# Performance work log

Hardware: AMD Instinct MI355X
Metric: run time of the kernel (lower is better)

The kernel has to match this reference:

```python
import jax, jax.numpy as jnp
import numpy as np

N = 50000
E = 1_600_000
D_IN = 128
D_H = 64
D_E = 32
NEG_SLOPE = 0.2


def setup_inputs() -> dict:
    key = jax.random.key(0)
    ks = jax.random.split(key, 20)
    p = lambda k, sh: jax.random.normal(k, sh, jnp.float32) * 0.1
    return {
        "x": jax.random.normal(ks[0], (N, D_IN), jnp.float32),
        "edge_index": jax.random.randint(ks[1], (2, E), 0, N, jnp.int32),
        "edge_attr": jax.random.normal(ks[2], (E, D_E), jnp.float32),
        # layer 1 params (GATv2Conv, heads=1)
        "Wl1": p(ks[3], (D_IN, D_H)), "bl1": p(ks[4], (D_H,)),
        "Wr1": p(ks[5], (D_IN, D_H)), "br1": p(ks[6], (D_H,)),
        "We1": p(ks[7], (D_E, D_H)),
        "att1": p(ks[8], (D_H,)), "bias1": p(ks[9], (D_H,)),
        # layer 2 params
        "Wl2": p(ks[10], (D_H, D_H)), "bl2": p(ks[11], (D_H,)),
        "Wr2": p(ks[12], (D_H, D_H)), "br2": p(ks[13], (D_H,)),
        "We2": p(ks[14], (D_E, D_H)),
        "att2": p(ks[15], (D_H,)), "bias2": p(ks[16], (D_H,)),
        # classifier
        "Wc": p(ks[17], (D_H, 2)), "bc": p(ks[18], (2,)),
    }


def _gatv2(x, src, dst, eattr, Wl, bl, Wr, br, We, att, bias, n):
    # x: [n, d_in]; src/dst: [Ea]; eattr: [Ea, d_e]
    xl = x @ Wl + bl                      # [n, d_h] (source transform; also message value)
    xr = x @ Wr + br                      # [n, d_h] (target transform)
    z = xl[src] + xr[dst] + eattr @ We    # [Ea, d_h]
    score = jax.nn.leaky_relu(z, NEG_SLOPE) @ att  # [Ea]
    # numerically stable softmax over incoming edges per destination node
    m = jax.ops.segment_max(score, dst, num_segments=n)
    ex = jnp.exp(score - m[dst])
    denom = jax.ops.segment_sum(ex, dst, num_segments=n)
    alpha = ex / denom[dst]               # [Ea]
    out = jax.ops.segment_sum(alpha[:, None] * xl[src], dst, num_segments=n)
    return out + bias


def reference(x, edge_index, edge_attr,
              Wl1, bl1, Wr1, br1, We1, att1, bias1,
              Wl2, bl2, Wr2, br2, We2, att2, bias2,
              Wc, bc):
    n = x.shape[0]
    src, dst = edge_index[0], edge_index[1]
    # add self-loops with fill_value='mean' (PyG default with edge_attr):
    # self-loop edge feature of node i = mean of edge_attr over edges into i
    e = edge_attr.shape[0]
    deg = jax.ops.segment_sum(jnp.ones((e,), edge_attr.dtype), dst, num_segments=n)
    loop_attr = jax.ops.segment_sum(edge_attr, dst, num_segments=n) / jnp.maximum(deg, 1.0)[:, None]
    loop = jnp.arange(n, dtype=edge_index.dtype)
    src_a = jnp.concatenate([src, loop])
    dst_a = jnp.concatenate([dst, loop])
    ea = jnp.concatenate([edge_attr, loop_attr], axis=0)

    h = jax.nn.relu(_gatv2(x, src_a, dst_a, ea, Wl1, bl1, Wr1, br1, We1, att1, bias1, n))
    # dropout(p=0.2) is identity in eval mode
    h = jax.nn.relu(_gatv2(h, src_a, dst_a, ea, Wl2, bl2, Wr2, br2, We2, att2, bias2, n))
    return h @ Wc + bc  # [n, 2]
```

## Files before the change

kernel.cpp:

```cpp
#include <hip/hip_runtime.h>
#include <hip/hip_bf16.h>

#define NEG_SLOPE 0.2f

__device__ __forceinline__ float bf2f(unsigned short u) {
    return __uint_as_float((unsigned)u << 16);
}
__device__ __forceinline__ unsigned short f2bf(float f) {
    unsigned b = __float_as_uint(f);
    return (unsigned short)((b + 0x7FFFu + ((b >> 16) & 1u)) >> 16);
}

__global__ void k_hist(const int* __restrict__ dst, int E, int* __restrict__ deg) {
    int e = blockIdx.x * 256 + threadIdx.x;
    if (e < E) atomicAdd(&deg[dst[e]], 1);
}

__global__ __launch_bounds__(1024) void k_scan_chunk(const int* __restrict__ deg,
                                                     int* __restrict__ start,
                                                     int* __restrict__ csum, int n) {
    __shared__ int wsum[16];
    const int lane = threadIdx.x & 63;
    const int w = threadIdx.x >> 6;
    int i = blockIdx.x * 1024 + (int)threadIdx.x;
    int v = (i < n) ? deg[i] : 0;
    int s = v;
#pragma unroll
    for (int o = 1; o < 64; o <<= 1) {
        int u = __shfl_up(s, o);
        if (lane >= o) s += u;
    }
    if (lane == 63) wsum[w] = s;
    __syncthreads();
    if (w == 0) {
        int ws = (lane < 16) ? wsum[lane] : 0;
#pragma unroll
        for (int o = 1; o < 16; o <<= 1) {
            int u = __shfl_up(ws, o);
            if (lane >= o) ws += u;
        }
        if (lane < 16) wsum[lane] = ws;
    }
    __syncthreads();
    int woff = (w == 0) ? 0 : wsum[w - 1];
    int incl = s + woff;
    if (i < n) start[i] = incl - v;
    if (threadIdx.x == 1023) csum[blockIdx.x] = incl;
}

__global__ void k_scan_top(int* __restrict__ csum, int nch, int* __restrict__ start, int n) {
    int t = threadIdx.x;
    int v = (t < nch) ? csum[t] : 0;
    int s = v;
#pragma unroll
    for (int o = 1; o < 64; o <<= 1) {
        int u = __shfl_up(s, o);
        if (t >= o) s += u;
    }
    if (t < nch) csum[t] = s - v;
    if (t == 63) start[n] = s;
}

__global__ void k_scan_apply(int* __restrict__ start, const int* __restrict__ csum, int n) {
    int i = blockIdx.x * 256 + threadIdx.x;
    if (i < n) start[i] += csum[i >> 10];
}

__global__ void k_fill(const int* __restrict__ src, const int* __restrict__ dst, int E,
                       const int* __restrict__ start, int* __restrict__ cursor,
                       int* __restrict__ perm, int* __restrict__ src_sorted,
                       int* __restrict__ sortpos) {
    int e = blockIdx.x * 256 + threadIdx.x;
    if (e >= E) return;
    int d = dst[e];
    int idx = start[d] + atomicAdd(&cursor[d], 1);
    perm[idx] = e;
    src_sorted[idx] = src[e];
    sortpos[e] = idx;
}

__global__ __launch_bounds__(256) void k_loop_csr(
    const float* __restrict__ eattr, const int* __restrict__ perm,
    const int* __restrict__ start, float* __restrict__ loop_attr, int n) {
    int node = blockIdx.x * 4 + (threadIdx.x >> 6);
    int t = threadIdx.x & 63;
    if (node >= n) return;
    int a = start[node], b = start[node + 1];
    int g = t >> 3, gl = t & 7;
    float4 acc = make_float4(0.f, 0.f, 0.f, 0.f);
    int j = a + g;
    for (; j + 8 < b; j += 16) {
        int e1 = perm[j];
        int e2 = perm[j + 8];
        const float4 v1 = *(const float4*)&eattr[(size_t)e1 * 32 + gl * 4];
        const float4 v2 = *(const float4*)&eattr[(size_t)e2 * 32 + gl * 4];
        acc.x += v1.x + v2.x; acc.y += v1.y + v2.y;
        acc.z += v1.z + v2.z; acc.w += v1.w + v2.w;
    }
    if (j < b) {
        int e = perm[j];
        const float4 v = *(const float4*)&eattr[(size_t)e * 32 + gl * 4];
        acc.x += v.x; acc.y += v.y; acc.z += v.z; acc.w += v.w;
    }
#pragma unroll
    for (int mask = 8; mask <= 32; mask <<= 1) {
        acc.x += __shfl_xor(acc.x, mask);
        acc.y += __shfl_xor(acc.y, mask);
        acc.z += __shfl_xor(acc.z, mask);
        acc.w += __shfl_xor(acc.w, mask);
    }
    if (t < 8) {
        float deg = fmaxf((float)(b - a), 1.f);
        float4 o = make_float4(acc.x / deg, acc.y / deg, acc.z / deg, acc.w / deg);
        *(float4*)&loop_attr[(size_t)node * 32 + gl * 4] = o;
    }
}

template <int DIN>
__global__ void k_node_transform(const float* __restrict__ h,
                                 const float* __restrict__ Wl, const float* __restrict__ bl,
                                 const float* __restrict__ Wr, const float* __restrict__ br,
                                 float* __restrict__ xl, unsigned short* __restrict__ xlb,
                                 unsigned short* __restrict__ xrb, int n) {
    __shared__ float hs[4][DIN];
    int node0 = blockIdx.x * 4;
    int tid = threadIdx.x;
    for (int idx = tid; idx < 4 * DIN; idx += 256) {
        int ln = idx / DIN, k = idx % DIN;
        int node = node0 + ln;
        hs[ln][k] = (node < n) ? h[(long long)node * DIN + k] : 0.f;
    }
    __syncthreads();
    int ln = tid >> 6;
    int j = tid & 63;
    int node = node0 + ln;
    if (node >= n) return;
    float al = bl[j], ar = br[j];
#pragma unroll 8
    for (int k = 0; k < DIN; ++k) {
        float hv = hs[ln][k];
        al += hv * Wl[k * 64 + j];
        ar += hv * Wr[k * 64 + j];
    }
    xl[(long long)node * 64 + j] = al;
    xlb[(long long)node * 64 + j] = f2bf(al);
    xrb[(long long)node * 64 + j] = f2bf(ar);
}

__global__ __launch_bounds__(256, 2) void k_edge_score(
    const unsigned short* __restrict__ xlb, const unsigned short* __restrict__ xrb,
    const float* __restrict__ eattr,
    const float* __restrict__ We, const float* __restrict__ att,
    const int* __restrict__ src, const int* __restrict__ dst,
    const int* __restrict__ sortpos, int E,
    float* __restrict__ ex_sorted) {
    __shared__ __align__(16) float We_s[32 * 64];
    __shared__ __align__(16) float ea_T[32][132];
    __shared__ float att_s[64];
    __shared__ int s_s[128], d_s[128], sp_s[128];

    const int tid = threadIdx.x;
    const int ge0 = blockIdx.x * 128;

    if (tid < 128) {
        int ge = ge0 + tid;
        bool ok = ge < E;
        s_s[tid] = ok ? src[ge] : 0;
        d_s[tid] = ok ? dst[ge] : 0;
        sp_s[tid] = ok ? sortpos[ge] : 0;
    }
    {
        const int e = tid & 127;
        const int kc = (tid >> 7) * 16;
        const int ge = ge0 + e;
        float4 a = make_float4(0.f, 0.f, 0.f, 0.f), b = a, c = a, d4 = a;
        if (ge < E) {
            const float4* p = (const float4*)(eattr + (size_t)ge * 32 + kc);
            a = p[0]; b = p[1]; c = p[2]; d4 = p[3];
        }
        ea_T[kc + 0][e] = a.x;  ea_T[kc + 1][e] = a.y;  ea_T[kc + 2][e] = a.z;  ea_T[kc + 3][e] = a.w;
        ea_T[kc + 4][e] = b.x;  ea_T[kc + 5][e] = b.y;  ea_T[kc + 6][e] = b.z;  ea_T[kc + 7][e] = b.w;
        ea_T[kc + 8][e] = c.x;  ea_T[kc + 9][e] = c.y;  ea_T[kc + 10][e] = c.z; ea_T[kc + 11][e] = c.w;
        ea_T[kc + 12][e] = d4.x; ea_T[kc + 13][e] = d4.y; ea_T[kc + 14][e] = d4.z; ea_T[kc + 15][e] = d4.w;
    }
    for (int i = tid; i < 2048; i += 256) We_s[i] = We[i];
    if (tid < 64) att_s[tid] = att[tid];
    __syncthreads();

    const int w = tid >> 6, l = tid & 63;
    const int t0 = (l & 15) * 4;
    const int e0 = w * 32 + (l >> 4) * 8;

    ushort4 xlv[8], xrv[8];
#pragma unroll
    for (int j = 0; j < 8; ++j) {
        const int eb = e0 + j;
        xlv[j] = *(const ushort4*)&xlb[(size_t)s_s[eb] * 64 + t0];
        xrv[j] = *(const ushort4*)&xrb[(size_t)d_s[eb] * 64 + t0];
    }

    float z[8][4];
#pragma unroll
    for (int j = 0; j < 8; ++j)
#pragma unroll
        for (int i = 0; i < 4; ++i) z[j][i] = 0.f;

#pragma unroll 4
    for (int k = 0; k < 32; ++k) {
        const float4 ev0 = *(const float4*)&ea_T[k][e0];
        const float4 ev1 = *(const float4*)&ea_T[k][e0 + 4];
        const float4 wv = *(const float4*)&We_s[k * 64 + t0];
        const float ee[8] = {ev0.x, ev0.y, ev0.z, ev0.w, ev1.x, ev1.y, ev1.z, ev1.w};
        const float ww[4] = {wv.x, wv.y, wv.z, wv.w};
#pragma unroll
        for (int j = 0; j < 8; ++j)
#pragma unroll
            for (int i = 0; i < 4; ++i) z[j][i] += ee[j] * ww[i];
    }

    const float4 av = *(const float4*)&att_s[t0];
    const float aa[4] = {av.x, av.y, av.z, av.w};
    float v[8];
#pragma unroll
    for (int j = 0; j < 8; ++j) {
        const float xll[4] = {bf2f(xlv[j].x), bf2f(xlv[j].y), bf2f(xlv[j].z), bf2f(xlv[j].w)};
        const float xrr[4] = {bf2f(xrv[j].x), bf2f(xrv[j].y), bf2f(xrv[j].z), bf2f(xrv[j].w)};
        float acc = 0.f;
#pragma unroll
        for (int i = 0; i < 4; ++i) {
            float zz = z[j][i] + xll[i] + xrr[i];
            zz = (zz > 0.f) ? zz : NEG_SLOPE * zz;
            acc += aa[i] * zz;
        }
        v[j] = acc;
    }
#pragma unroll
    for (int m = 1; m < 16; m <<= 1) {
#pragma unroll
        for (int j = 0; j < 8; ++j) v[j] += __shfl_xor(v[j], m);
    }
    if ((l & 15) == 0) {
#pragma unroll
        for (int j = 0; j < 8; ++j) {
            int ge = ge0 + e0 + j;
            if (ge < E) ex_sorted[sp_s[e0 + j]] = __expf(v[j]);
        }
    }
}

__global__ __launch_bounds__(256) void k_loop_score(
    const unsigned short* __restrict__ xlb, const unsigned short* __restrict__ xrb,
    const float* __restrict__ loop_attr,
    const float* __restrict__ We, const float* __restrict__ att,
    int n, float* __restrict__ ex_loop) {
    __shared__ float We_s[32 * 64];
    __shared__ float ea_T[32][68];
    __shared__ float att_s[64];

    const int tid = threadIdx.x;
    const int ge0 = blockIdx.x * 64;

    for (int i = tid; i < 2048; i += 256) We_s[i] = We[i];
    if (tid < 64) att_s[tid] = att[tid];
    {
        int e = tid & 63;
        int k0 = (tid >> 6) * 8;
        int ge = ge0 + e;
        float4 a = make_float4(0.f, 0.f, 0.f, 0.f), b = a;
        if (ge < n) {
            const float4* p = (const float4*)(loop_attr + (size_t)ge * 32 + k0);
            a = p[0]; b = p[1];
        }
        ea_T[k0 + 0][e] = a.x; ea_T[k0 + 1][e] = a.y; ea_T[k0 + 2][e] = a.z; ea_T[k0 + 3][e] = a.w;
        ea_T[k0 + 4][e] = b.x; ea_T[k0 + 5][e] = b.y; ea_T[k0 + 6][e] = b.z; ea_T[k0 + 7][e] = b.w;
    }
    __syncthreads();

    const int w = tid >> 6, l = tid & 63;
    const int t0 = (l & 15) * 4;
    const int e0 = w * 16 + (l >> 4) * 4;

    float z[4][4];
#pragma unroll
    for (int j = 0; j < 4; ++j)
#pragma unroll
        for (int i = 0; i < 4; ++i) z[j][i] = 0.f;

#pragma unroll 8
    for (int k = 0; k < 32; ++k) {
        const float4 ev = *(const float4*)&ea_T[k][e0];
        const float4 wv = *(const float4*)&We_s[k * 64 + t0];
        const float ee[4] = {ev.x, ev.y, ev.z, ev.w};
        const float ww[4] = {wv.x, wv.y, wv.z, wv.w};
#pragma unroll
        for (int j = 0; j < 4; ++j)
#pragma unroll
            for (int i = 0; i < 4; ++i) z[j][i] += ee[j] * ww[i];
    }

    const float4 av = *(const float4*)&att_s[t0];
    const float aa[4] = {av.x, av.y, av.z, av.w};
    float v[4];
#pragma unroll
    for (int j = 0; j < 4; ++j) {
        const int node = ge0 + e0 + j;
        const int nsafe = (node < n) ? node : 0;
        const ushort4 xlv = *(const ushort4*)&xlb[(size_t)nsafe * 64 + t0];
        const ushort4 xrv = *(const ushort4*)&xrb[(size_t)nsafe * 64 + t0];
        const float xll[4] = {bf2f(xlv.x), bf2f(xlv.y), bf2f(xlv.z), bf2f(xlv.w)};
        const float xrr[4] = {bf2f(xrv.x), bf2f(xrv.y), bf2f(xrv.z), bf2f(xrv.w)};
        float acc = 0.f;
#pragma unroll
        for (int i = 0; i < 4; ++i) {
            float zz = z[j][i] + xll[i] + xrr[i];
            zz = (zz > 0.f) ? zz : NEG_SLOPE * zz;
            acc += aa[i] * zz;
        }
        v[j] = acc;
    }
#pragma unroll
    for (int m = 1; m < 16; m <<= 1) {
#pragma unroll
        for (int j = 0; j < 4; ++j) v[j] += __shfl_xor(v[j], m);
    }
    if ((l & 15) == 0) {
#pragma unroll
        for (int j = 0; j < 4; ++j) {
            int node = ge0 + e0 + j;
            if (node < n) ex_loop[node] = __expf(v[j]);
        }
    }
}

template <bool FINAL>
__global__ __launch_bounds__(256, 2) void k_node_aggr(
    const float* __restrict__ xl, const int* __restrict__ start,
    const int* __restrict__ src_sorted, const float* __restrict__ ex_sorted,
    const float* __restrict__ ex_loop, const float* __restrict__ bias,
    const float* __restrict__ Wc, const float* __restrict__ bc,
    float* __restrict__ hout, int n) {
    int node = blockIdx.x * 4 + (threadIdx.x >> 6);
    int t = threadIdx.x & 63;
    if (node >= n) return;
    const int es = t >> 4;
    const int cg = t & 15;
    int a = start[node], b = start[node + 1];

    float4 acc = make_float4(0.f, 0.f, 0.f, 0.f);
    float den = 0.f;
    if (es == 0) {
        float exl = ex_loop[node];
        const float4 xv = *(const float4*)&xl[(size_t)node * 64 + cg * 4];
        acc.x = exl * xv.x; acc.y = exl * xv.y; acc.z = exl * xv.z; acc.w = exl * xv.w;
        den = exl;
    }
    for (int j = a; j < b; j += 64) {
        int m = b - j; if (m > 64) m = 64;
        int sj = 0; float exj = 0.f;
        if (t < m) { sj = src_sorted[j + t]; exj = ex_sorted[j + t]; }
        for (int i = 0; i < m; i += 16) {
            int idx[4]; float ex4[4]; const float4* p4[4];
#pragma unroll
            for (int q = 0; q < 4; ++q) {
                idx[q] = i + q * 4 + es;
                const int sq = __shfl(sj, idx[q]);
                ex4[q] = __shfl(exj, idx[q]);
                p4[q] = (const float4*)&xl[(size_t)sq * 64 + cg * 4];
            }
            float4 xv[4];
#pragma unroll
            for (int q = 0; q < 4; ++q)
                xv[q] = (idx[q] < m) ? *p4[q] : make_float4(0.f, 0.f, 0.f, 0.f);
#pragma unroll
            for (int q = 0; q < 4; ++q) {
                const float eq = (idx[q] < m) ? ex4[q] : 0.f;
                acc.x += eq * xv[q].x; acc.y += eq * xv[q].y;
                acc.z += eq * xv[q].z; acc.w += eq * xv[q].w;
                den += eq;
            }
        }
    }
#pragma unroll
    for (int mask = 16; mask <= 32; mask <<= 1) {
        acc.x += __shfl_xor(acc.x, mask);
        acc.y += __shfl_xor(acc.y, mask);
        acc.z += __shfl_xor(acc.z, mask);
        acc.w += __shfl_xor(acc.w, mask);
        den   += __shfl_xor(den, mask);
    }
    if (!FINAL) {
        if (es == 0) {
            const float4 bv = *(const float4*)&bias[cg * 4];
            float4 h;
            h.x = fmaxf(acc.x / den + bv.x, 0.f);
            h.y = fmaxf(acc.y / den + bv.y, 0.f);
            h.z = fmaxf(acc.z / den + bv.z, 0.f);
            h.w = fmaxf(acc.w / den + bv.w, 0.f);
            *(float4*)&hout[(size_t)node * 64 + cg * 4] = h;
        }
    } else {
        float v0 = 0.f, v1 = 0.f;
        if (es == 0) {
            const float4 bv = *(const float4*)&bias[cg * 4];
            const float h0 = fmaxf(acc.x / den + bv.x, 0.f);
            const float h1 = fmaxf(acc.y / den + bv.y, 0.f);
            const float h2 = fmaxf(acc.z / den + bv.z, 0.f);
            const float h3 = fmaxf(acc.w / den + bv.w, 0.f);
            const int c0 = cg * 4;
            v0 = h0 * Wc[(c0 + 0) * 2 + 0] + h1 * Wc[(c0 + 1) * 2 + 0]
               + h2 * Wc[(c0 + 2) * 2 + 0] + h3 * Wc[(c0 + 3) * 2 + 0];
            v1 = h0 * Wc[(c0 + 0) * 2 + 1] + h1 * Wc[(c0 + 1) * 2 + 1]
               + h2 * Wc[(c0 + 2) * 2 + 1] + h3 * Wc[(c0 + 3) * 2 + 1];
        }
#pragma unroll
        for (int mask = 1; mask <= 8; mask <<= 1) {
            v0 += __shfl_xor(v0, mask);
            v1 += __shfl_xor(v1, mask);
        }
        if (t == 0) {
            hout[(size_t)node * 2 + 0] = v0 + bc[0];
            hout[(size_t)node * 2 + 1] = v1 + bc[1];
        }
    }
}

extern "C" void kernel_launch(void* const* d_in, const int* in_sizes, int n_in,
                              void* d_out, int out_size, void* d_ws, size_t ws_size,
                              hipStream_t stream) {
    const float* x     = (const float*)d_in[0];
    const int*   ei    = (const int*)d_in[1];
    const float* eattr = (const float*)d_in[2];
    const float* Wl1 = (const float*)d_in[3];
    const float* bl1 = (const float*)d_in[4];
    const float* Wr1 = (const float*)d_in[5];
    const float* br1 = (const float*)d_in[6];
    const float* We1 = (const float*)d_in[7];
    const float* att1 = (const float*)d_in[8];
    const float* bias1 = (const float*)d_in[9];
    const float* Wl2 = (const float*)d_in[10];
    const float* bl2 = (const float*)d_in[11];
    const float* Wr2 = (const float*)d_in[12];
    const float* br2 = (const float*)d_in[13];
    const float* We2 = (const float*)d_in[14];
    const float* att2 = (const float*)d_in[15];
    const float* bias2 = (const float*)d_in[16];
    const float* Wc = (const float*)d_in[17];
    const float* bc = (const float*)d_in[18];

    const int N = in_sizes[0] / 128;
    const int E = in_sizes[1] / 2;
    const int* src = ei;
    const int* dst = ei + E;

    char* w = (char*)d_ws;
    auto alloc = [&](size_t bytes) {
        char* p = w;
        w += (bytes + 255) & ~(size_t)255;
        return p;
    };
    float*          xl         = (float*)alloc((size_t)N * 64 * 4);
    unsigned short* xlb        = (unsigned short*)alloc((size_t)N * 64 * 2);
    unsigned short* xrb        = (unsigned short*)alloc((size_t)N * 64 * 2);
    float*          hbuf       = (float*)alloc((size_t)N * 64 * 4);
    float*          loop_attr  = (float*)alloc((size_t)N * 32 * 4);
    float*          ex_loop    = (float*)alloc((size_t)N * 4);
    int*            deg_i      = (int*)alloc((size_t)N * 4);
    int*            start      = (int*)alloc((size_t)(N + 1) * 4);
    int*            cursor     = (int*)alloc((size_t)N * 4);
    int*            csum       = (int*)alloc(256 * 4);
    int*            perm       = (int*)alloc((size_t)E * 4);
    int*            src_sorted = (int*)alloc((size_t)E * 4);
    int*            sortpos    = (int*)alloc((size_t)E * 4);
    float*          ex_sorted  = (float*)alloc((size_t)E * 4);

    const int THREADS = 256;
    const int score_blocks = (E + 127) / 128;
    const int loop_blocks = (N + 63) / 64;
    const int node4_blocks = (N + 3) / 4;
    const int edge_blocks = (E + THREADS - 1) / THREADS;
    const int nchunks = (N + 1023) / 1024;

    hipMemsetAsync(deg_i, 0, (size_t)N * 4, stream);
    hipMemsetAsync(cursor, 0, (size_t)N * 4, stream);
    k_hist<<<edge_blocks, THREADS, 0, stream>>>(dst, E, deg_i);
    k_scan_chunk<<<nchunks, 1024, 0, stream>>>(deg_i, start, csum, N);
    k_scan_top<<<1, 64, 0, stream>>>(csum, nchunks, start, N);
    k_scan_apply<<<(N + THREADS - 1) / THREADS, THREADS, 0, stream>>>(start, csum, N);
    k_fill<<<edge_blocks, THREADS, 0, stream>>>(src, dst, E, start, cursor,
                                                perm, src_sorted, sortpos);
    k_loop_csr<<<node4_blocks, THREADS, 0, stream>>>(eattr, perm, start, loop_attr, N);

    k_node_transform<128><<<node4_blocks, THREADS, 0, stream>>>(x, Wl1, bl1, Wr1, br1,
                                                                xl, xlb, xrb, N);
    k_edge_score<<<score_blocks, THREADS, 0, stream>>>(
        xlb, xrb, eattr, We1, att1, src, dst, sortpos, E, ex_sorted);
    k_loop_score<<<loop_blocks, THREADS, 0, stream>>>(xlb, xrb, loop_attr, We1, att1, N, ex_loop);
    k_node_aggr<false><<<node4_blocks, THREADS, 0, stream>>>(xl, start, src_sorted, ex_sorted,
                                                             ex_loop, bias1, Wc, bc, hbuf, N);

    k_node_transform<64><<<node4_blocks, THREADS, 0, stream>>>(hbuf, Wl2, bl2, Wr2, br2,
                                                               xl, xlb, xrb, N);
    k_loop_score<<<loop_blocks, THREADS, 0, stream>>>(xlb, xrb, loop_attr, We2, att2, N, ex_loop);
    k_edge_score<<<score_blocks, THREADS, 0, stream>>>(
        xlb, xrb, eattr, We2, att2, src, dst, sortpos, E, ex_sorted);
    k_node_aggr<true><<<node4_blocks, THREADS, 0, stream>>>(xl, start, src_sorted, ex_sorted,
                                                            ex_loop, bias2, Wc, bc, (float*)d_out, N);
}
```

Baseline: 767.7 us.

## Compute edge-attribute projection in edge score kernel with bf16 MFMA

Replaces the scalar FMA loop computing eattr@We per edge with 16x16x32 bf16 MFMA instructions, staging edge attributes in LDS as bf16 fragments and loading We directly into register fragments. The output layout is remapped so each lane handles one edge and four channels per tile, with a two-step shuffle reduction for the attention dot product. This cuts ALU work and shared-memory footprint in the score kernel at the cost of reduced precision for the edge term.

```diff
diff --git a/kernel.cpp b/kernel.cpp
--- a/kernel.cpp
+++ b/kernel.cpp
@@ -2,6 +2,9 @@
 #include <hip/hip_bf16.h>
 
 #define NEG_SLOPE 0.2f
+
+typedef __attribute__((ext_vector_type(8))) short bf16x8;
+typedef __attribute__((ext_vector_type(4))) float f32x4;
 
 __device__ __forceinline__ float bf2f(unsigned short u) {
     return __uint_as_float((unsigned)u << 16);
@@ -154,8 +157,7 @@
     const int* __restrict__ src, const int* __restrict__ dst,
     const int* __restrict__ sortpos, int E,
     float* __restrict__ ex_sorted) {
-    __shared__ __align__(16) float We_s[32 * 64];
-    __shared__ __align__(16) float ea_T[32][132];
+    __shared__ __align__(16) short ea_frag[4][128][8];
     __shared__ float att_s[64];
     __shared__ int s_s[128], d_s[128], sp_s[128];
 
@@ -169,81 +171,82 @@
         d_s[tid] = ok ? dst[ge] : 0;
         sp_s[tid] = ok ? sortpos[ge] : 0;
     }
+    if (tid >= 128 && tid < 192) att_s[tid - 128] = att[tid - 128];
     {
         const int e = tid & 127;
-        const int kc = (tid >> 7) * 16;
+        const int c0 = (tid >> 7) * 2;
         const int ge = ge0 + e;
         float4 a = make_float4(0.f, 0.f, 0.f, 0.f), b = a, c = a, d4 = a;
         if (ge < E) {
-            const float4* p = (const float4*)(eattr + (size_t)ge * 32 + kc);
+            const float4* p = (const float4*)(eattr + (size_t)ge * 32 + c0 * 8);
             a = p[0]; b = p[1]; c = p[2]; d4 = p[3];
         }
-        ea_T[kc + 0][e] = a.x;  ea_T[kc + 1][e] = a.y;  ea_T[kc + 2][e] = a.z;  ea_T[kc + 3][e] = a.w;
-        ea_T[kc + 4][e] = b.x;  ea_T[kc + 5][e] = b.y;  ea_T[kc + 6][e] = b.z;  ea_T[kc + 7][e] = b.w;
-        ea_T[kc + 8][e] = c.x;  ea_T[kc + 9][e] = c.y;  ea_T[kc + 10][e] = c.z; ea_T[kc + 11][e] = c.w;
-        ea_T[kc + 12][e] = d4.x; ea_T[kc + 13][e] = d4.y; ea_T[kc + 14][e] = d4.z; ea_T[kc + 15][e] = d4.w;
-    }
-    for (int i = tid; i < 2048; i += 256) We_s[i] = We[i];
-    if (tid < 64) att_s[tid] = att[tid];
+        bf16x8 lo, hi;
+        lo[0] = (short)f2bf(a.x); lo[1] = (short)f2bf(a.y); lo[2] = (short)f2bf(a.z); lo[3] = (short)f2bf(a.w);
+        lo[4] = (short)f2bf(b.x); lo[5] = (short)f2bf(b.y); lo[6] = (short)f2bf(b.z); lo[7] = (short)f2bf(b.w);
+        hi[0] = (short)f2bf(c.x); hi[1] = (short)f2bf(c.y); hi[2] = (short)f2bf(c.z); hi[3] = (short)f2bf(c.w);
+        hi[4] = (short)f2bf(d4.x); hi[5] = (short)f2bf(d4.y); hi[6] = (short)f2bf(d4.z); hi[7] = (short)f2bf(d4.w);
+        *(bf16x8*)&ea_frag[c0 + 0][e][0] = lo;
+        *(bf16x8*)&ea_frag[c0 + 1][e][0] = hi;
+    }
+
+    const int w = tid >> 6, l = tid & 63;
+    const int lo16 = l & 15, hi4 = l >> 4;
+
+    bf16x8 afrag[4];
+#pragma unroll
+    for (int ct = 0; ct < 4; ++ct) {
+#pragma unroll
+        for (int j = 0; j < 8; ++j) {
+            afrag[ct][j] = (short)f2bf(We[(hi4 * 8 + j) * 64 + ct * 16 + lo16]);
+        }
+    }
     __syncthreads();
 
-    const int w = tid >> 6, l = tid & 63;
-    const int t0 = (l & 15) * 4;
-    const int e0 = w * 32 + (l >> 4) * 8;
-
-    ushort4 xlv[8], xrv[8];
-#pragma unroll
-    for (int j = 0; j < 8; ++j) {
-        const int eb = e0 + j;
-        xlv[j] = *(const ushort4*)&xlb[(size_t)s_s[eb] * 64 + t0];
-        xrv[j] = *(const ushort4*)&xrb[(size_t)d_s[eb] * 64 + t0];
-    }
-
-    float z[8][4];
-#pragma unroll
-    for (int j = 0; j < 8; ++j)
-#pragma unroll
-        for (int i = 0; i < 4; ++i) z[j][i] = 0.f;
-
-#pragma unroll 4
-    for (int k = 0; k < 32; ++k) {
-        const float4 ev0 = *(const float4*)&ea_T[k][e0];
-        const float4 ev1 = *(const float4*)&ea_T[k][e0 + 4];
-        const float4 wv = *(const float4*)&We_s[k * 64 + t0];
-        const float ee[8] = {ev0.x, ev0.y, ev0.z, ev0.w, ev1.x, ev1.y, ev1.z, ev1.w};
-        const float ww[4] = {wv.x, wv.y, wv.z, wv.w};
-#pragma unroll
-        for (int j = 0; j < 8; ++j)
-#pragma unroll
-            for (int i = 0; i < 4; ++i) z[j][i] += ee[j] * ww[i];
-    }
-
-    const float4 av = *(const float4*)&att_s[t0];
-    const float aa[4] = {av.x, av.y, av.z, av.w};
-    float v[8];
-#pragma unroll
-    for (int j = 0; j < 8; ++j) {
-        const float xll[4] = {bf2f(xlv[j].x), bf2f(xlv[j].y), bf2f(xlv[j].z), bf2f(xlv[j].w)};
-        const float xrr[4] = {bf2f(xrv[j].x), bf2f(xrv[j].y), bf2f(xrv[j].z), bf2f(xrv[j].w)};
-        float acc = 0.f;
-#pragma unroll
-        for (int i = 0; i < 4; ++i) {
-            float zz = z[j][i] + xll[i] + xrr[i];
-            zz = (zz > 0.f) ? zz : NEG_SLOPE * zz;
-            acc += aa[i] * zz;
-        }
-        v[j] = acc;
-    }
-#pragma unroll
-    for (int m = 1; m < 16; m <<= 1) {
-#pragma unroll
-        for (int j = 0; j < 8; ++j) v[j] += __shfl_xor(v[j], m);
-    }
-    if ((l & 15) == 0) {
-#pragma unroll
-        for (int j = 0; j < 8; ++j) {
-            int ge = ge0 + e0 + j;
-            if (ge < E) ex_sorted[sp_s[e0 + j]] = __expf(v[j]);
+    const int base_e0 = w * 32;
+
+    f32x4 acc[2][4];
+#pragma unroll
+    for (int et = 0; et < 2; ++et) {
+        const int base_e = base_e0 + et * 16;
+        bf16x8 bfrag = *(const bf16x8*)&ea_frag[hi4][base_e + lo16][0];
+#pragma unroll
+        for (int ct = 0; ct < 4; ++ct) {
+            f32x4 zero = {0.f, 0.f, 0.f, 0.f};
+            acc[et][ct] = __builtin_amdgcn_mfma_f32_16x16x32_bf16(afrag[ct], bfrag, zero, 0, 0, 0);
+        }
+    }
+
+    float attr_[4][4];
+#pragma unroll
+    for (int ct = 0; ct < 4; ++ct) {
+        const float4 av = *(const float4*)&att_s[ct * 16 + hi4 * 4];
+        attr_[ct][0] = av.x; attr_[ct][1] = av.y; attr_[ct][2] = av.z; attr_[ct][3] = av.w;
+    }
+
+#pragma unroll
+    for (int et = 0; et < 2; ++et) {
+        const int eb = base_e0 + et * 16 + lo16;
+        const int s = s_s[eb], d = d_s[eb];
+        float part = 0.f;
+#pragma unroll
+        for (int ct = 0; ct < 4; ++ct) {
+            const ushort4 xlv = *(const ushort4*)&xlb[(size_t)s * 64 + ct * 16 + hi4 * 4];
+            const ushort4 xrv = *(const ushort4*)&xrb[(size_t)d * 64 + ct * 16 + hi4 * 4];
+            const float xll[4] = {bf2f(xlv.x), bf2f(xlv.y), bf2f(xlv.z), bf2f(xlv.w)};
+            const float xrr[4] = {bf2f(xrv.x), bf2f(xrv.y), bf2f(xrv.z), bf2f(xrv.w)};
+#pragma unroll
+            for (int r = 0; r < 4; ++r) {
+                float zz = acc[et][ct][r] + xll[r] + xrr[r];
+                zz = (zz > 0.f) ? zz : NEG_SLOPE * zz;
+                part += attr_[ct][r] * zz;
+            }
+        }
+        part += __shfl_xor(part, 16);
+        part += __shfl_xor(part, 32);
+        if (l < 16) {
+            int ge = ge0 + base_e0 + et * 16 + l;
+            if (ge < E) ex_sorted[sp_s[base_e0 + et * 16 + l]] = __expf(part);
         }
     }
 }
```

Result: slower. 805.5 us (+4.9%).
